# Kernel optimization log

Measured on AMD Instinct MI355X. Metric: run time of the kernel, lower is better.

## Reference

```python
import jax, jax.numpy as jnp
import numpy as np
import itertools, math

B, T, D = 4, 4096, 1024
H = 16
DIM = D // H          # 64
L, KB = 8, 4
R = 1 << KB           # 16
S = L * R             # 128
TOPK = 2


def setup_inputs() -> dict:
    key = jax.random.key(0)
    ks = jax.random.split(key, 8)
    x = jax.random.normal(ks[0], (B, T, D), dtype=jnp.float32)
    mask = jnp.ones((B, T), dtype=jnp.float32)
    sc = 1.0 / math.sqrt(D)
    Wq = jax.random.normal(ks[1], (D, D), dtype=jnp.float32) * sc
    Wk = jax.random.normal(ks[2], (D, D), dtype=jnp.float32) * sc
    Wv = jax.random.normal(ks[3], (D, D), dtype=jnp.float32) * sc
    Wout = jax.random.normal(ks[4], (D, D), dtype=jnp.float32) * sc
    b_out = jnp.zeros((D,), dtype=jnp.float32)
    # planes: (L, K_bits, head_dim) -> stored transposed as (head_dim, L*K_bits)
    planes = jax.random.normal(ks[5], (L * KB, DIM), dtype=jnp.float32)
    planes_T = planes.T
    # hypercube corners (R, K_bits) -> stored transposed as (K_bits, R)
    corners = jnp.asarray(list(itertools.product([-1.0, 1.0], repeat=KB)), dtype=jnp.float32)
    protos_T = corners.T
    logit_temp = jnp.zeros((), dtype=jnp.float32)  # log(1.0)
    return {"x": x, "mask": mask, "Wq": Wq, "Wk": Wk, "Wv": Wv,
            "Wout": Wout, "b_out": b_out, "planes_T": planes_T,
            "protos_T": protos_T, "logit_temp": logit_temp}


def reference(x, mask, Wq, Wk, Wv, Wout, b_out, planes_T, protos_T, logit_temp):
    b, t, d = x.shape
    Q = (x @ Wq).reshape(b, t, H, DIM)
    K = (x @ Wk).reshape(b, t, H, DIM)
    V = (x @ Wv).reshape(b, t, H, DIM)
    m = mask[:, :, None, None]
    Q, K, V = Q * m, K * m, V * m
    Q = jnp.transpose(Q, (0, 2, 1, 3))  # [B,H,T,dim]
    K = jnp.transpose(K, (0, 2, 1, 3))
    V = jnp.transpose(V, (0, 2, 1, 3))

    scale = jnp.clip(jnp.exp(logit_temp), 0.01, 20.0)
    # LSH hyperplane projections of K
    projK = jnp.einsum('bhtd,dp->bhtp', K, planes_T).reshape(b, H, t, L, KB)
    logitsK = jnp.einsum('bhtlk,kr->bhtlr', jnp.tanh(projK) / scale, protos_T)
    probsK = jax.nn.softmax(logitsK, axis=-1)  # [B,H,T,L,R]

    # top-k mask over R, then renormalize
    _, top_idx = jax.lax.top_k(probsK, TOPK)
    sel = jax.nn.one_hot(top_idx, R, dtype=probsK.dtype).sum(axis=-2)
    probsK = probsK * sel
    probsK = probsK / (probsK.sum(axis=-1, keepdims=True) + 1e-6)

    assign = probsK.reshape(b, H, t, S)  # [B,H,T,S]
    bucket_K = jnp.einsum('bhts,bhtd->bhsd', assign, K)
    bucket_V = jnp.einsum('bhts,bhtd->bhsd', assign, V)
    A = assign.sum(axis=2)[..., None]  # [B,H,S,1]
    bucket_K = bucket_K / (A + 1e-6)
    bucket_V = bucket_V / (A + 1e-6)

    scores = jnp.einsum('bhtd,bhsd->bhts', Q, bucket_K) / math.sqrt(DIM)
    probs_attn = jax.nn.softmax(scores, axis=-1)
    out = jnp.einsum('bhts,bhsd->bhtd', probs_attn, bucket_V)
    out = jnp.transpose(out, (0, 2, 1, 3)).reshape(b, t, d)
    return out @ Wout + b_out
```

## Files before the change

kernel.cpp:

```cpp
#include <hip/hip_runtime.h>
#include <math.h>
#include <stdint.h>

#define TT   4096
#define DD   1024
#define HH   16
#define DIMM 64
#define SS   128

typedef short bf16x8 __attribute__((ext_vector_type(8)));
typedef float f32x4  __attribute__((ext_vector_type(4)));

__device__ __forceinline__ unsigned short f2bf(float f) {
    uint32_t u = __float_as_uint(f);
    return (unsigned short)((u + 0x7fffu + ((u >> 16) & 1u)) >> 16);
}
__device__ __forceinline__ float bf2f(unsigned short h) {
    return __uint_as_float((uint32_t)h << 16);
}

#define GLD16(ldsp, gp) __builtin_amdgcn_global_load_lds( \
    (const __attribute__((address_space(1))) uint32_t*)(gp), \
    (__attribute__((address_space(3))) uint32_t*)(ldsp), 16, 0, 0)

__global__ __launch_bounds__(256) void cvt2_k(const float* __restrict__ x,
                                              unsigned short* __restrict__ xb,
                                              unsigned short* __restrict__ xlo)
{
    const size_t i = ((size_t)blockIdx.x * 256 + threadIdx.x) * 8;
    const float4 a = *(const float4*)&x[i];
    const float4 b = *(const float4*)&x[i + 4];
    const float v[8] = {a.x, a.y, a.z, a.w, b.x, b.y, b.z, b.w};
    unsigned short h[8], l[8];
#pragma unroll
    for (int j = 0; j < 8; j++) {
        h[j] = f2bf(v[j]);
        l[j] = f2bf(v[j] - bf2f(h[j]));
    }
    uint4 rh, rl;
    rh.x = (uint32_t)h[0] | ((uint32_t)h[1] << 16);
    rh.y = (uint32_t)h[2] | ((uint32_t)h[3] << 16);
    rh.z = (uint32_t)h[4] | ((uint32_t)h[5] << 16);
    rh.w = (uint32_t)h[6] | ((uint32_t)h[7] << 16);
    rl.x = (uint32_t)l[0] | ((uint32_t)l[1] << 16);
    rl.y = (uint32_t)l[2] | ((uint32_t)l[3] << 16);
    rl.z = (uint32_t)l[4] | ((uint32_t)l[5] << 16);
    rl.w = (uint32_t)l[6] | ((uint32_t)l[7] << 16);
    *(uint4*)&xb[i]  = rh;
    *(uint4*)&xlo[i] = rl;
}

__global__ __launch_bounds__(256) void tr_k(const float* __restrict__ W,
                                            unsigned short* __restrict__ WT)
{
    __shared__ unsigned short tile[32][33];
    const int bx = blockIdx.x * 32;
    const int by = blockIdx.y * 32;
    const int tx = threadIdx.x & 31, ty = threadIdx.x >> 5;
#pragma unroll
    for (int r = 0; r < 4; r++) {
        const int row = by + ty * 4 + r;
        tile[tx][ty * 4 + r] = f2bf(W[(size_t)row * 1024 + bx + tx]);
    }
    __syncthreads();
#pragma unroll
    for (int r = 0; r < 4; r++) {
        const int col = bx + ty * 4 + r;
        WT[(size_t)col * 1024 + by + tx] = tile[ty * 4 + r][tx];
    }
}

__global__ __launch_bounds__(256) void tr2_k(const float* __restrict__ Wp,
                                             unsigned short* __restrict__ WphT,
                                             unsigned short* __restrict__ WplT)
{
    __shared__ float tile[32][33];
    const int bx = blockIdx.x * 32;
    const int by = blockIdx.y * 32;
    const int tx = threadIdx.x & 31, ty = threadIdx.x >> 5;
#pragma unroll
    for (int r = 0; r < 4; r++) {
        const int row = by + ty * 4 + r;
        tile[tx][ty * 4 + r] = Wp[(size_t)row * 512 + bx + tx];
    }
    __syncthreads();
#pragma unroll
    for (int r = 0; r < 4; r++) {
        const int col = bx + ty * 4 + r;
        const float v = tile[ty * 4 + r][tx];
        const unsigned short hi = f2bf(v);
        const unsigned short lo = f2bf(v - bf2f(hi));
        WphT[(size_t)col * 1024 + by + tx] = hi;
        WplT[(size_t)col * 1024 + by + tx] = lo;
    }
}

__global__ __launch_bounds__(256) void qkv_k(
    const unsigned short* __restrict__ Abf, const unsigned short* __restrict__ BT,
    const float* __restrict__ mask, unsigned short* __restrict__ Qf,
    unsigned short* __restrict__ KVf)
{
    __shared__ short sMem[16384];
    short* sA = sMem;
    short* sB = sMem + 8192;
    const int tid = threadIdx.x;
    const int w  = tid >> 6;
    const int ln = tid & 63;
    const int wm = w & 1, wn = w >> 1;
    const int id   = blockIdx.y * 24 + blockIdx.x;
    const int xcd  = id & 7, kk = id >> 3;
    const int cg   = kk / 192, rem = kk % 192;
    const int band = xcd * 16 + rem / 12;
    const int colblk = cg * 12 + rem % 12;
    const int row0 = band * 128;
    const int col0 = colblk * 128;
    const int lr = ln >> 4, lc = ln & 15;

    f32x4 acc[4][4];
#pragma unroll
    for (int i = 0; i < 4; i++)
#pragma unroll
        for (int j = 0; j < 4; j++) acc[i][j] = (f32x4){0.f, 0.f, 0.f, 0.f};

    const int ia0 = 2 * w, ia1 = 2 * w + 1;
    const size_t gA0 = (size_t)(row0 + ia0 * 16 + lc) * 1024 + lr * 8;
    const size_t gA1 = (size_t)(row0 + ia1 * 16 + lc) * 1024 + lr * 8;
    const size_t gB0 = (size_t)(col0 + ia0 * 16 + lc) * 1024 + lr * 8;
    const size_t gB1 = (size_t)(col0 + ia1 * 16 + lc) * 1024 + lr * 8;

    auto STAGE = [&](int buf, int k0) {
        GLD16(&sA[buf * 4096 + ia0 * 512], Abf + gA0 + k0);
        GLD16(&sA[buf * 4096 + ia1 * 512], Abf + gA1 + k0);
        GLD16(&sB[buf * 4096 + ia0 * 512], BT  + gB0 + k0);
        GLD16(&sB[buf * 4096 + ia1 * 512], BT  + gB1 + k0);
    };

    STAGE(0, 0);
    __syncthreads();
    for (int t = 0; t < 32; t++) {
        const int cur = t & 1;
        if (t < 31) STAGE(cur ^ 1, (t + 1) * 32);
        bf16x8 af[4], bfr[4];
#pragma unroll
        for (int ib = 0; ib < 4; ib++)
            af[ib] = *(const bf16x8*)&sA[cur * 4096 + (wm * 4 + ib) * 512 + ln * 8];
#pragma unroll
        for (int jb = 0; jb < 4; jb++)
            bfr[jb] = *(const bf16x8*)&sB[cur * 4096 + (wn * 4 + jb) * 512 + ln * 8];
#pragma unroll
        for (int ib = 0; ib < 4; ib++)
#pragma unroll
            for (int jb = 0; jb < 4; jb++)
                acc[ib][jb] = __builtin_amdgcn_mfma_f32_16x16x32_bf16(
                    af[ib], bfr[jb], acc[ib][jb], 0, 0, 0);
        __syncthreads();
    }

    const int proj = colblk >> 3;
    const int b    = row0 >> 12;
    const int h0   = (colblk & 7) * 2;
    short* sT = sMem;

    if (proj == 0) {
#pragma unroll
        for (int ib = 0; ib < 4; ib++) {
#pragma unroll
            for (int r = 0; r < 4; r++) {
                const int tt = wm * 64 + ib * 16 + lr * 4 + r;
                const float mval = mask[row0 + tt];
#pragma unroll
                for (int jb = 0; jb < 4; jb++) {
                    const int d = jb * 16 + lc;
                    const int e = ((tt >> 4) * 2 + (d >> 5)) * 512 +
                                  ((tt & 15) + ((d >> 3) & 3) * 16) * 8 + (d & 7);
                    sT[wn * 8192 + e] = (short)f2bf(acc[ib][jb][r] * mval);
                }
            }
        }
        __syncthreads();
        const int tile = (row0 & (TT - 1)) >> 7;
#pragma unroll
        for (int i = 0; i < 8; i++) {
            const int flat = i * 256 + tid;
            const int h_l  = flat >> 10;
            const int off  = (flat & 1023) * 8;
            unsigned short* dst = Qf + (size_t)(b * HH + h0 + h_l) * 262144
                                + (size_t)tile * 8192 + off;
            *(uint4*)dst = *(const uint4*)&sT[h_l * 8192 + off];
        }
    } else {
        const int voff = (proj == 2) ? 4 : 0;
#pragma unroll
        for (int ib = 0; ib < 4; ib++) {
#pragma unroll
            for (int r = 0; r < 4; r++) {
                const int tt128 = wm * 64 + ib * 16 + lr * 4 + r;
                const float mval = mask[row0 + tt128];
                const int chunk = tt128 >> 6, tt6 = tt128 & 63;
                const int rbase = (wn * 2 + chunk) * 4096 +
                                  ((tt6 >> 3) & 3) * 128 + lc * 8 + (tt6 & 7);
                const int t5 = (tt6 >> 5) * 4 * 512;
#pragma unroll
                for (int jb = 0; jb < 4; jb++)
                    sT[rbase + t5 + jb * 512] = (short)f2bf(acc[ib][jb][r] * mval);
            }
        }
        __syncthreads();
        const int gc0 = (row0 & (TT - 1)) >> 6;
#pragma unroll
        for (int i = 0; i < 8; i++) {
            const int flat = i * 256 + tid;
            const int bf = flat >> 6;
            const int wi = flat & 63;
            const int h_l = bf >> 4, chunk = (bf >> 3) & 1;
            const int tt5 = (bf >> 2) & 1, nb = bf & 3;
            const int lidx = (h_l * 2 + chunk) * 4096 + (tt5 * 4 + nb) * 512 + wi * 8;
            const size_t gidx = (size_t)(b * HH + h0 + h_l) * 524288
                              + (size_t)(gc0 + chunk) * 8192
                              + (size_t)(tt5 * 8 + nb + voff) * 512 + wi * 8;
            *(uint4*)&KVf[gidx] = *(const uint4*)&sT[lidx];
        }
    }
}

__global__ __launch_bounds__(256) void out_k(
    const unsigned short* __restrict__ Abf, const unsigned short* __restrict__ BT,
    const float* __restrict__ bias, float* __restrict__ C)
{
    __shared__ short sA[2][4096];
    __shared__ short sB[2][4096];
    const int tid = threadIdx.x;
    const int w  = tid >> 6, ln = tid & 63;
    const int wm = w & 1, wn = w >> 1;
    const int id  = blockIdx.y * 8 + blockIdx.x;
    const int xcd = id & 7, kk = id >> 3;
    const int row0 = (xcd * 16 + (kk >> 3)) * 128;
    const int col0 = (kk & 7) * 128;
    const int lr = ln >> 4, lc = ln & 15;

    f32x4 acc[4][4];
#pragma unroll
    for (int i = 0; i < 4; i++)
#pragma unroll
        for (int j = 0; j < 4; j++) acc[i][j] = (f32x4){0.f, 0.f, 0.f, 0.f};

    const int ia0 = 2 * w, ia1 = 2 * w + 1;
    const size_t gA0 = (size_t)(row0 + ia0 * 16 + lc) * 1024 + lr * 8;
    const size_t gA1 = (size_t)(row0 + ia1 * 16 + lc) * 1024 + lr * 8;
    const size_t gB0 = (size_t)(col0 + ia0 * 16 + lc) * 1024 + lr * 8;
    const size_t gB1 = (size_t)(col0 + ia1 * 16 + lc) * 1024 + lr * 8;

    auto STAGE = [&](int buf, int k0) {
        GLD16(&sA[buf][ia0 * 512], Abf + gA0 + k0);
        GLD16(&sA[buf][ia1 * 512], Abf + gA1 + k0);
        GLD16(&sB[buf][ia0 * 512], BT  + gB0 + k0);
        GLD16(&sB[buf][ia1 * 512], BT  + gB1 + k0);
    };

    STAGE(0, 0);
    __syncthreads();
    for (int t = 0; t < 32; t++) {
        const int cur = t & 1;
        if (t < 31) STAGE(cur ^ 1, (t + 1) * 32);
        bf16x8 af[4], bfr[4];
#pragma unroll
        for (int ib = 0; ib < 4; ib++)
            af[ib] = *(const bf16x8*)&sA[cur][(wm * 4 + ib) * 512 + ln * 8];
#pragma unroll
        for (int jb = 0; jb < 4; jb++)
            bfr[jb] = *(const bf16x8*)&sB[cur][(wn * 4 + jb) * 512 + ln * 8];
#pragma unroll
        for (int ib = 0; ib < 4; ib++)
#pragma unroll
            for (int jb = 0; jb < 4; jb++)
                acc[ib][jb] = __builtin_amdgcn_mfma_f32_16x16x32_bf16(
                    af[ib], bfr[jb], acc[ib][jb], 0, 0, 0);
        __syncthreads();
    }

#pragma unroll
    for (int ib = 0; ib < 4; ib++) {
#pragma unroll
        for (int r = 0; r < 4; r++) {
            const int gr = row0 + wm * 64 + ib * 16 + lr * 4 + r;
#pragma unroll
            for (int jb = 0; jb < 4; jb++) {
                const int col = col0 + wn * 64 + jb * 16 + lc;
                C[(size_t)gr * 1024 + col] = acc[ib][jb][r] + bias[col];
            }
        }
    }
}

__global__ __launch_bounds__(256) void projm_k(
    const unsigned short* __restrict__ Ah, const unsigned short* __restrict__ Al,
    const unsigned short* __restrict__ Bh, const unsigned short* __restrict__ Bl,
    const float* __restrict__ mask, float* __restrict__ P)
{
    __shared__ short sAh[2][4096];
    __shared__ short sAl[2][4096];
    __shared__ short sBh[2][4096];
    __shared__ short sBl[2][4096];
    const int tid = threadIdx.x;
    const int w  = tid >> 6;
    const int ln = tid & 63;
    const int wm = w & 1, wn = w >> 1;
    const int id  = blockIdx.y * 4 + blockIdx.x;
    const int xcd = id & 7, kk = id >> 3;
    const int row0 = (xcd * 16 + (kk >> 2)) * 128;
    const int col0 = (kk & 3) * 128;
    const int lr = ln >> 4, lc = ln & 15;

    f32x4 acc[4][4];
#pragma unroll
    for (int i = 0; i < 4; i++)
#pragma unroll
        for (int j = 0; j < 4; j++) acc[i][j] = (f32x4){0.f, 0.f, 0.f, 0.f};

    const int ia0 = 2 * w, ia1 = 2 * w + 1;
    const size_t gA0 = (size_t)(row0 + ia0 * 16 + lc) * 1024 + lr * 8;
    const size_t gA1 = (size_t)(row0 + ia1 * 16 + lc) * 1024 + lr * 8;
    const size_t gB0 = (size_t)(col0 + ia0 * 16 + lc) * 1024 + lr * 8;
    const size_t gB1 = (size_t)(col0 + ia1 * 16 + lc) * 1024 + lr * 8;

    auto STAGE = [&](int buf, int k0) {
        GLD16(&sAh[buf][ia0 * 512], Ah + gA0 + k0);
        GLD16(&sAh[buf][ia1 * 512], Ah + gA1 + k0);
        GLD16(&sAl[buf][ia0 * 512], Al + gA0 + k0);
        GLD16(&sAl[buf][ia1 * 512], Al + gA1 + k0);
        GLD16(&sBh[buf][ia0 * 512], Bh + gB0 + k0);
        GLD16(&sBh[buf][ia1 * 512], Bh + gB1 + k0);
        GLD16(&sBl[buf][ia0 * 512], Bl + gB0 + k0);
        GLD16(&sBl[buf][ia1 * 512], Bl + gB1 + k0);
    };

    STAGE(0, 0);
    __syncthreads();
    for (int t = 0; t < 32; t++) {
        const int cur = t & 1;
        if (t < 31) STAGE(cur ^ 1, (t + 1) * 32);
        bf16x8 ah[4], al[4], bh[4], bl[4];
#pragma unroll
        for (int ib = 0; ib < 4; ib++) {
            ah[ib] = *(const bf16x8*)&sAh[cur][(wm * 4 + ib) * 512 + ln * 8];
            al[ib] = *(const bf16x8*)&sAl[cur][(wm * 4 + ib) * 512 + ln * 8];
        }
#pragma unroll
        for (int jb = 0; jb < 4; jb++) {
            bh[jb] = *(const bf16x8*)&sBh[cur][(wn * 4 + jb) * 512 + ln * 8];
            bl[jb] = *(const bf16x8*)&sBl[cur][(wn * 4 + jb) * 512 + ln * 8];
        }
#pragma unroll
        for (int ib = 0; ib < 4; ib++)
#pragma unroll
            for (int jb = 0; jb < 4; jb++) {
                acc[ib][jb] = __builtin_amdgcn_mfma_f32_16x16x32_bf16(
                    ah[ib], bh[jb], acc[ib][jb], 0, 0, 0);
                acc[ib][jb] = __builtin_amdgcn_mfma_f32_16x16x32_bf16(
                    ah[ib], bl[jb], acc[ib][jb], 0, 0, 0);
                acc[ib][jb] = __builtin_amdgcn_mfma_f32_16x16x32_bf16(
                    al[ib], bh[jb], acc[ib][jb], 0, 0, 0);
            }
        __syncthreads();
    }

#pragma unroll
    for (int ib = 0; ib < 4; ib++) {
#pragma unroll
        for (int r = 0; r < 4; r++) {
            const int gr = row0 + wm * 64 + ib * 16 + lr * 4 + r;
            const float mval = mask[gr];
            const int b = gr >> 12, t = gr & (TT - 1);
#pragma unroll
            for (int jb = 0; jb < 4; jb++) {
                const int c = col0 + wn * 64 + jb * 16 + lc;
                const int h = c >> 5, p = c & 31;
                P[(((size_t)(b * HH + h) * TT + t) * 32) + p] =
                    acc[ib][jb][r] * mval;
            }
        }
    }
}

__global__ __launch_bounds__(256) void wproj_k(
    const float* __restrict__ Wk, const float* __restrict__ planesT,
    float* __restrict__ Wp)
{
    __shared__ float sW[1024];
    __shared__ float sP[2048];
    const int tid = threadIdx.x;
    const int k = blockIdx.x;
    for (int i = tid; i < 1024; i += 256) sW[i] = Wk[(size_t)k * 1024 + i];
    for (int i = tid; i < 2048; i += 256) sP[i] = planesT[i];
    __syncthreads();
#pragma unroll
    for (int c0 = 0; c0 < 2; c0++) {
        const int c = c0 * 256 + tid;
        const int h = c >> 5, p = c & 31;
        float s = 0.f;
#pragma unroll
        for (int d = 0; d < 64; d++)
            s = fmaf(sW[h * 64 + d], sP[d * 32 + p], s);
        Wp[(size_t)k * 512 + c] = s;
    }
}

__global__ __launch_bounds__(256) void zero_k(float* __restrict__ p)
{
    const size_t i = ((size_t)blockIdx.x * 256 + threadIdx.x) * 4;
    *(float4*)&p[i] = make_float4(0.f, 0.f, 0.f, 0.f);
}

__global__ __launch_bounds__(256) void assign_k(
    const float* __restrict__ Pj, const float* __restrict__ protosT,
    const float* __restrict__ logit_temp,
    unsigned char* __restrict__ aIdx, float* __restrict__ aW,
    float* __restrict__ gA)
{
    __shared__ float sPr[4][16];
    __shared__ float sCnt[SS];
    const int tid = threadIdx.x;
    const int tc = blockIdx.x;
    const int bh = blockIdx.y;

    if (tid < 64)  ((float*)sPr)[tid] = protosT[tid];
    if (tid < SS)  sCnt[tid] = 0.f;
    __syncthreads();

    const float scale = fminf(fmaxf(__expf(logit_temp[0]), 0.01f), 20.0f);
    const float inv_scale = 1.0f / scale;

    const int t = tc * 256 + tid;
    const float* pr = Pj + ((size_t)bh * TT + t) * 32;
    float proj[32];
#pragma unroll
    for (int j = 0; j < 8; j++) {
        const float4 v = *(const float4*)&pr[j * 4];
        proj[j * 4 + 0] = v.x; proj[j * 4 + 1] = v.y;
        proj[j * 4 + 2] = v.z; proj[j * 4 + 3] = v.w;
    }
#pragma unroll
    for (int p = 0; p < 32; p++) proj[p] = tanhf(proj[p]) * inv_scale;

    unsigned char idx[16];
    float wv[16];
#pragma unroll
    for (int l = 0; l < 8; l++) {
        float g[16];
#pragma unroll
        for (int r = 0; r < 16; r++)
            g[r] = proj[l * 4 + 0] * sPr[0][r] + proj[l * 4 + 1] * sPr[1][r] +
                   proj[l * 4 + 2] * sPr[2][r] + proj[l * 4 + 3] * sPr[3][r];
        float mx = g[0];
#pragma unroll
        for (int r = 1; r < 16; r++) mx = fmaxf(mx, g[r]);
        float Zs = 0.f;
#pragma unroll
        for (int r = 0; r < 16; r++) Zs += __expf(g[r] - mx);
        int a = 0; float ga = g[0];
#pragma unroll
        for (int r = 1; r < 16; r++) { if (g[r] > ga) { ga = g[r]; a = r; } }
        int b2 = (a == 0) ? 1 : 0; float gb = g[b2];
#pragma unroll
        for (int r = 0; r < 16; r++) { if (r != a && g[r] > gb) { gb = g[r]; b2 = r; } }
        const float pa = __expf(ga - mx) / Zs;
        const float pb = __expf(gb - mx) / Zs;
        const float den = pa + pb + 1e-6f;
        const float wa = pa / den, wb = pb / den;
        idx[l * 2 + 0] = (unsigned char)(l * 16 + a);  wv[l * 2 + 0] = wa;
        idx[l * 2 + 1] = (unsigned char)(l * 16 + b2); wv[l * 2 + 1] = wb;
        atomicAdd(&sCnt[l * 16 + a],  wa);
        atomicAdd(&sCnt[l * 16 + b2], wb);
    }
    const size_t off = (size_t)bh * TT + t;
    uint32_t pk[4];
#pragma unroll
    for (int j = 0; j < 4; j++)
        pk[j] = (uint32_t)idx[j * 4] | ((uint32_t)idx[j * 4 + 1] << 8) |
                ((uint32_t)idx[j * 4 + 2] << 16) | ((uint32_t)idx[j * 4 + 3] << 24);
    *(uint4*)&aIdx[off * 16] = make_uint4(pk[0], pk[1], pk[2], pk[3]);
#pragma unroll
    for (int j = 0; j < 4; j++)
        *(float4*)&aW[off * 16 + j * 4] =
            make_float4(wv[j * 4], wv[j * 4 + 1], wv[j * 4 + 2], wv[j * 4 + 3]);
    __syncthreads();
    if (tid < SS) atomicAdd(&gA[bh * SS + tid], sCnt[tid]);
}

__global__ __launch_bounds__(256) void scatter4_k(
    const unsigned short* __restrict__ KVf,
    const unsigned char* __restrict__ aIdx, const float* __restrict__ aW,
    float* __restrict__ gBK, float* __restrict__ gBV)
{
    __shared__ short sA[8192];
    __shared__ short sB[8192];
    const int tid = threadIdx.x;
    const int tc = blockIdx.x;
    const int bh = blockIdx.y;
    const int w  = tid >> 6, ln = tid & 63;
    const int wm = w & 1, wn = w >> 1;

    f32x4 acc[4][4];
#pragma unroll
    for (int i = 0; i < 4; i++)
#pragma unroll
        for (int j = 0; j < 4; j++) acc[i][j] = (f32x4){0.f, 0.f, 0.f, 0.f};

    const size_t kvbase = (size_t)bh * 524288;
    const int ptt = tid >> 2, pg = tid & 3;

    for (int c = 0; c < 8; c++) {
        __syncthreads();
        const size_t cbase = kvbase + (size_t)(tc * 8 + c) * 8192;
#pragma unroll
        for (int i = 0; i < 4; i++) {
            const int seg = w * 4 + i;
            GLD16(&sB[seg * 512], KVf + cbase + seg * 512 + ln * 8);
        }
        {
            const uint4 z = make_uint4(0u, 0u, 0u, 0u);
#pragma unroll
            for (int r = 0; r < 4; r++)
                *(uint4*)&sA[(r * 256 + tid) * 8] = z;
        }
        __syncthreads();
        {
            const int t0 = tc * 512 + c * 64;
            const size_t off = (size_t)bh * TT + (t0 + ptt);
            const uint32_t pk = ((const uint32_t*)aIdx)[off * 4 + pg];
            const float4 wv = *(const float4*)&aW[off * 16 + pg * 4];
            const float w4[4] = {wv.x, wv.y, wv.z, wv.w};
#pragma unroll
            for (int q = 0; q < 4; q++) {
                const int s = (pk >> (8 * q)) & 255;
                sA[((ptt >> 5) * 8 + (s >> 4)) * 512 + ((ptt >> 3) & 3) * 128 +
                   (s & 15) * 8 + (ptt & 7)] = f2bf(w4[q]);
            }
        }
        __syncthreads();
#pragma unroll
        for (int ks = 0; ks < 2; ks++) {
            bf16x8 af[4], bfr[4];
#pragma unroll
            for (int ib = 0; ib < 4; ib++)
                af[ib] = *(const bf16x8*)&sA[(ks * 8 + wm * 4 + ib) * 512 + ln * 8];
#pragma unroll
            for (int jb = 0; jb < 4; jb++)
                bfr[jb] = *(const bf16x8*)&sB[(ks * 8 + wn * 4 + jb) * 512 + ln * 8];
#pragma unroll
            for (int ib = 0; ib < 4; ib++)
#pragma unroll
                for (int jb = 0; jb < 4; jb++)
                    acc[ib][jb] = __builtin_amdgcn_mfma_f32_16x16x32_bf16(
                        af[ib], bfr[jb], acc[ib][jb], 0, 0, 0);
        }
    }

    const int lr = ln >> 4, lc = ln & 15;
#pragma unroll
    for (int ib = 0; ib < 4; ib++) {
#pragma unroll
        for (int r = 0; r < 4; r++) {
            const int s = wm * 64 + ib * 16 + lr * 4 + r;
#pragma unroll
            for (int jb = 0; jb < 4; jb++) {
                const int col = wn * 64 + jb * 16 + lc;
                if (col < 64)
                    atomicAdd(&gBK[(size_t)bh * (SS * DIMM) + s * DIMM + col],
                              acc[ib][jb][r]);
                else
                    atomicAdd(&gBV[(size_t)bh * (SS * DIMM) + s * DIMM + (col - 64)],
                              acc[ib][jb][r]);
            }
        }
    }
}

__global__ __launch_bounds__(256) void bprep_k(
    const float* __restrict__ gBK, const float* __restrict__ gBV,
    const float* __restrict__ gA,
    unsigned short* __restrict__ Kf, unsigned short* __restrict__ VTf)
{
    __shared__ float sInv[SS];
    const int tid = threadIdx.x;
    const int bh = blockIdx.y;
    if (tid < SS) sInv[tid] = 1.0f / (gA[bh * SS + tid] + 1e-6f);
    __syncthreads();
#pragma unroll
    for (int it = 0; it < 8; it++) {
        const int i = (blockIdx.x * 8 + it) * 256 + tid;
        const int s = i >> 6, d = i & 63;
        const float kv = gBK[(size_t)bh * 8192 + i] * sInv[s];
        const float vv = gBV[(size_t)bh * 8192 + i] * sInv[s];
        const int ek = ((s >> 4) * 2 + (d >> 5)) * 512 +
                       ((s & 15) + ((d >> 3) & 3) * 16) * 8 + (d & 7);
        const int ev = ((d >> 4) * 4 + (s >> 5)) * 512 +
                       ((d & 15) + ((s >> 3) & 3) * 16) * 8 + (s & 7);
        Kf[(size_t)bh * 8192 + ek]  = f2bf(kv);
        VTf[(size_t)bh * 8192 + ev] = f2bf(vv);
    }
}

__global__ __launch_bounds__(256) void attn_m(
    const unsigned short* __restrict__ Qf, const unsigned short* __restrict__ Kf,
    const unsigned short* __restrict__ VTf, unsigned short* __restrict__ attb)
{
    __shared__ short sQ[8192];
    __shared__ short sK[8192];
    __shared__ short sVT[8192];
    __shared__ short sP[16384];
    const int tid = threadIdx.x;
    const int tc = blockIdx.x;
    const int bh = blockIdx.y;
    const int w = tid >> 6, l = tid & 63;

    const size_t qbase  = (size_t)bh * 262144 + (size_t)tc * 8192;
    const size_t kvbase = (size_t)bh * 8192;
#pragma unroll
    for (int i = 0; i < 4; i++) {
        const int o = (i * 256 + w * 64) * 8;
        GLD16(&sQ[o],  Qf  + qbase  + o + l * 8);
        GLD16(&sK[o],  Kf  + kvbase + o + l * 8);
        GLD16(&sVT[o], VTf + kvbase + o + l * 8);
    }
    __syncthreads();

    f32x4 acc[2][8];
#pragma unroll
    for (int i = 0; i < 2; i++)
#pragma unroll
        for (int j = 0; j < 8; j++) acc[i][j] = (f32x4){0.f, 0.f, 0.f, 0.f};

#pragma unroll
    for (int ks = 0; ks < 2; ks++) {
        const bf16x8 a0 = *(const bf16x8*)&sQ[((w * 2 + 0) * 2 + ks) * 512 + l * 8];
        const bf16x8 a1 = *(const bf16x8*)&sQ[((w * 2 + 1) * 2 + ks) * 512 + l * 8];
#pragma unroll
        for (int jb = 0; jb < 8; jb++) {
            const bf16x8 b = *(const bf16x8*)&sK[(jb * 2 + ks) * 512 + l * 8];
            acc[0][jb] = __builtin_amdgcn_mfma_f32_16x16x32_bf16(a0, b, acc[0][jb], 0, 0, 0);
            acc[1][jb] = __builtin_amdgcn_mfma_f32_16x16x32_bf16(a1, b, acc[1][jb], 0, 0, 0);
        }
    }

#pragma unroll
    for (int ib = 0; ib < 2; ib++) {
        const int mb = w * 2 + ib;
#pragma unroll
        for (int r = 0; r < 4; r++) {
            float v[8];
            float mx = -INFINITY;
#pragma unroll
            for (int jb = 0; jb < 8; jb++) {
                v[jb] = acc[ib][jb][r] * 0.125f;
                mx = fmaxf(mx, v[jb]);
            }
            mx = fmaxf(mx, __shfl_xor(mx, 1));
            mx = fmaxf(mx, __shfl_xor(mx, 2));
            mx = fmaxf(mx, __shfl_xor(mx, 4));
            mx = fmaxf(mx, __shfl_xor(mx, 8));
            float Z = 0.f;
#pragma unroll
            for (int jb = 0; jb < 8; jb++) { v[jb] = __expf(v[jb] - mx); Z += v[jb]; }
            Z += __shfl_xor(Z, 1);
            Z += __shfl_xor(Z, 2);
            Z += __shfl_xor(Z, 4);
            Z += __shfl_xor(Z, 8);
            const float invZ = 1.0f / Z;
            const int ttl = (l >> 4) * 4 + r;
#pragma unroll
            for (int jb = 0; jb < 8; jb++) {
                int e = (mb * 4 + (jb >> 1)) * 512 +
                        (ttl + (((jb * 2 + ((l >> 3) & 1)) & 3) * 16)) * 8 + (l & 7);
                e ^= ((e >> 7) & 3) << 4;
                sP[e] = (short)f2bf(v[jb] * invZ);
            }
        }
    }

    f32x4 acc2[2][4];
#pragma unroll
    for (int i = 0; i < 2; i++)
#pragma unroll
        for (int j = 0; j < 4; j++) acc2[i][j] = (f32x4){0.f, 0.f, 0.f, 0.f};

#pragma unroll
    for (int ks = 0; ks < 4; ks++) {
        bf16x8 a[2];
#pragma unroll
        for (int ib = 0; ib < 2; ib++) {
            int ia = ((w * 2 + ib) * 4 + ks) * 512 + l * 8;
            ia ^= ((ia >> 7) & 3) << 4;
            a[ib] = *(const bf16x8*)&sP[ia];
        }
#pragma unroll
        for (int jb = 0; jb < 4; jb++) {
            const bf16x8 b = *(const bf16x8*)&sVT[(jb * 4 + ks) * 512 + l * 8];
            acc2[0][jb] = __builtin_amdgcn_mfma_f32_16x16x32_bf16(a[0], b, acc2[0][jb], 0, 0, 0);
            acc2[1][jb] = __builtin_amdgcn_mfma_f32_16x16x32_bf16(a[1], b, acc2[1][jb], 0, 0, 0);
        }
    }

    const int b = bh >> 4, h = bh & 15;
#pragma unroll
    for (int ib = 0; ib < 2; ib++) {
#pragma unroll
        for (int r = 0; r < 4; r++) {
            const int t = tc * 128 + w * 32 + ib * 16 + (l >> 4) * 4 + r;
            unsigned short* outp = attb + ((size_t)(b * TT + t)) * DD + h * DIMM;
#pragma unroll
            for (int jb = 0; jb < 4; jb++)
                outp[jb * 16 + (l & 15)] = f2bf(acc2[ib][jb][r]);
        }
    }
}

extern "C" void kernel_launch(void* const* d_in, const int* in_sizes, int n_in,
                              void* d_out, int out_size, void* d_ws, size_t ws_size,
                              hipStream_t stream)
{
    const float* x       = (const float*)d_in[0];
    const float* mask    = (const float*)d_in[1];
    const float* Wq      = (const float*)d_in[2];
    const float* Wk      = (const float*)d_in[3];
    const float* Wv      = (const float*)d_in[4];
    const float* Wout    = (const float*)d_in[5];
    const float* b_out   = (const float*)d_in[6];
    const float* planesT = (const float*)d_in[7];
    const float* protosT = (const float*)d_in[8];
    const float* ltemp   = (const float*)d_in[9];
    float* out = (float*)d_out;

    float* ws  = (float*)d_ws;
    float* gBK = ws + (3u << 24);
    float* gBV = gBK + 524288;
    float* gA  = gBV + 524288;
    unsigned short* Qf    = (unsigned short*)ws;
    unsigned short* BTall = (unsigned short*)(ws + (1u << 24));
    unsigned short* KVf   = (unsigned short*)(ws + (2u << 24));
    unsigned short* xlo   = KVf;
    unsigned short* xb    = (unsigned short*)(ws + 51388416);
    float*          Wp    = ws;
    unsigned short* WphT  = (unsigned short*)(ws + 524288);
    unsigned short* WplT  = (unsigned short*)(ws + 786432);
    float*          aW    = ws + 51388416;
    unsigned char*  aIdx  = (unsigned char*)(ws + 55582720);
    unsigned short* Kf    = (unsigned short*)(ws + 56631296);
    unsigned short* VTf   = (unsigned short*)(ws + 56893440);
    unsigned short* attb  = KVf;
    unsigned short* WoutT = (unsigned short*)(ws + 41943040);
    float*          Pj    = (float*)d_out;

    const dim3 tg(32, 32);
    const dim3 t2g(16, 32);
    const dim3 pg(4, 128);
    const dim3 qg(24, 128);
    const dim3 og(8, 128);

    cvt2_k<<<8192, 256, 0, stream>>>(x, xb, xlo);

    wproj_k<<<1024, 256, 0, stream>>>(Wk, planesT, Wp);
    tr2_k<<<t2g, 256, 0, stream>>>(Wp, WphT, WplT);
    projm_k<<<pg, 256, 0, stream>>>(xb, xlo, WphT, WplT, mask, Pj);

    tr_k<<<tg, 256, 0, stream>>>(Wq, BTall);
    tr_k<<<tg, 256, 0, stream>>>(Wk, BTall + 1048576);
    tr_k<<<tg, 256, 0, stream>>>(Wv, BTall + 2097152);
    qkv_k<<<qg, 256, 0, stream>>>(xb, BTall, mask, Qf, KVf);

    zero_k<<<1032, 256, 0, stream>>>(gBK);
    assign_k<<<dim3(16, 64), 256, 0, stream>>>(Pj, protosT, ltemp, aIdx, aW, gA);
    scatter4_k<<<dim3(8, 64), 256, 0, stream>>>(KVf, aIdx, aW, gBK, gBV);

    bprep_k<<<dim3(4, 64), 256, 0, stream>>>(gBK, gBV, gA, Kf, VTf);
    tr_k<<<tg, 256, 0, stream>>>(Wout, WoutT);
    attn_m<<<dim3(32, 64), 256, 0, stream>>>(Qf, Kf, VTf, attb);

    out_k<<<og, 256, 0, stream>>>(attb, WoutT, b_out, out);
}
```

Measured before the change: 629.9 us.

## Triple-buffer GEMM LDS staging with partial vmcnt waits in qkv and out kernels

Replaces the double-buffered K-loop in the QKV and output projection GEMMs with a three-stage ring buffer. Two tiles are kept in flight, and each iteration waits only for the oldest loads (vmcnt(4)) followed by a raw s_barrier instead of a full __syncthreads. The goal is to hide more global-to-LDS latency behind the MFMA work. The cost is 48KB of LDS per block, which may lower occupancy, plus redundant dummy loads in the final iterations.

```diff
diff --git a/kernel.cpp b/kernel.cpp
--- a/kernel.cpp
+++ b/kernel.cpp
@@ -100,9 +100,7 @@
     const float* __restrict__ mask, unsigned short* __restrict__ Qf,
     unsigned short* __restrict__ KVf)
 {
-    __shared__ short sMem[16384];
-    short* sA = sMem;
-    short* sB = sMem + 8192;
+    __shared__ short sMem[24576];
     const int tid = threadIdx.x;
     const int w  = tid >> 6;
     const int ln = tid & 63;
@@ -129,32 +127,37 @@
     const size_t gB1 = (size_t)(col0 + ia1 * 16 + lc) * 1024 + lr * 8;
 
     auto STAGE = [&](int buf, int k0) {
-        GLD16(&sA[buf * 4096 + ia0 * 512], Abf + gA0 + k0);
-        GLD16(&sA[buf * 4096 + ia1 * 512], Abf + gA1 + k0);
-        GLD16(&sB[buf * 4096 + ia0 * 512], BT  + gB0 + k0);
-        GLD16(&sB[buf * 4096 + ia1 * 512], BT  + gB1 + k0);
+        short* bb = sMem + buf * 8192;
+        GLD16(&bb[ia0 * 512], Abf + gA0 + k0);
+        GLD16(&bb[ia1 * 512], Abf + gA1 + k0);
+        GLD16(&bb[4096 + ia0 * 512], BT + gB0 + k0);
+        GLD16(&bb[4096 + ia1 * 512], BT + gB1 + k0);
     };
 
     STAGE(0, 0);
-    __syncthreads();
+    STAGE(1, 32);
+    asm volatile("s_waitcnt vmcnt(4)" ::: "memory");
+    __builtin_amdgcn_s_barrier();
     for (int t = 0; t < 32; t++) {
-        const int cur = t & 1;
-        if (t < 31) STAGE(cur ^ 1, (t + 1) * 32);
+        STAGE((t + 2) % 3, (t + 2 < 32) ? (t + 2) * 32 : 0);
+        const short* bb = sMem + (t % 3) * 8192;
         bf16x8 af[4], bfr[4];
 #pragma unroll
         for (int ib = 0; ib < 4; ib++)
-            af[ib] = *(const bf16x8*)&sA[cur * 4096 + (wm * 4 + ib) * 512 + ln * 8];
+            af[ib] = *(const bf16x8*)&bb[(wm * 4 + ib) * 512 + ln * 8];
 #pragma unroll
         for (int jb = 0; jb < 4; jb++)
-            bfr[jb] = *(const bf16x8*)&sB[cur * 4096 + (wn * 4 + jb) * 512 + ln * 8];
+            bfr[jb] = *(const bf16x8*)&bb[4096 + (wn * 4 + jb) * 512 + ln * 8];
 #pragma unroll
         for (int ib = 0; ib < 4; ib++)
 #pragma unroll
             for (int jb = 0; jb < 4; jb++)
                 acc[ib][jb] = __builtin_amdgcn_mfma_f32_16x16x32_bf16(
                     af[ib], bfr[jb], acc[ib][jb], 0, 0, 0);
-        __syncthreads();
-    }
+        asm volatile("s_waitcnt vmcnt(4)" ::: "memory");
+        __builtin_amdgcn_s_barrier();
+    }
+    __syncthreads();
 
     const int proj = colblk >> 3;
     const int b    = row0 >> 12;
@@ -227,8 +230,7 @@
     const unsigned short* __restrict__ Abf, const unsigned short* __restrict__ BT,
     const float* __restrict__ bias, float* __restrict__ C)
 {
-    __shared__ short sA[2][4096];
-    __shared__ short sB[2][4096];
+    __shared__ short sMem[24576];
     const int tid = threadIdx.x;
     const int w  = tid >> 6, ln = tid & 63;
     const int wm = w & 1, wn = w >> 1;
@@ -251,31 +253,35 @@
     const size_t gB1 = (size_t)(col0 + ia1 * 16 + lc) * 1024 + lr * 8;
 
     auto STAGE = [&](int buf, int k0) {
-        GLD16(&sA[buf][ia0 * 512], Abf + gA0 + k0);
-        GLD16(&sA[buf][ia1 * 512], Abf + gA1 + k0);
-        GLD16(&sB[buf][ia0 * 512], BT  + gB0 + k0);
-        GLD16(&sB[buf][ia1 * 512], BT  + gB1 + k0);
+        short* bb = sMem + buf * 8192;
+        GLD16(&bb[ia0 * 512], Abf + gA0 + k0);
+        GLD16(&bb[ia1 * 512], Abf + gA1 + k0);
+        GLD16(&bb[4096 + ia0 * 512], BT + gB0 + k0);
+        GLD16(&bb[4096 + ia1 * 512], BT + gB1 + k0);
     };
 
     STAGE(0, 0);
-    __syncthreads();
+    STAGE(1, 32);
+    asm volatile("s_waitcnt vmcnt(4)" ::: "memory");
+    __builtin_amdgcn_s_barrier();
     for (int t = 0; t < 32; t++) {
-        const int cur = t & 1;
-        if (t < 31) STAGE(cur ^ 1, (t + 1) * 32);
+        STAGE((t + 2) % 3, (t + 2 < 32) ? (t + 2) * 32 : 0);
+        const short* bb = sMem + (t % 3) * 8192;
         bf16x8 af[4], bfr[4];
 #pragma unroll
         for (int ib = 0; ib < 4; ib++)
-            af[ib] = *(const bf16x8*)&sA[cur][(wm * 4 + ib) * 512 + ln * 8];
+            af[ib] = *(const bf16x8*)&bb[(wm * 4 + ib) * 512 + ln * 8];
 #pragma unroll
         for (int jb = 0; jb < 4; jb++)
-            bfr[jb] = *(const bf16x8*)&sB[cur][(wn * 4 + jb) * 512 + ln * 8];
+            bfr[jb] = *(const bf16x8*)&bb[4096 + (wn * 4 + jb) * 512 + ln * 8];
 #pragma unroll
         for (int ib = 0; ib < 4; ib++)
 #pragma unroll
             for (int jb = 0; jb < 4; jb++)
                 acc[ib][jb] = __builtin_amdgcn_mfma_f32_16x16x32_bf16(
                     af[ib], bfr[jb], acc[ib][jb], 0, 0, 0);
-        __syncthreads();
+        asm volatile("s_waitcnt vmcnt(4)" ::: "memory");
+        __builtin_amdgcn_s_barrier();
     }
 
 #pragma unroll
```

Result: faster. 617.2 us (-2.0%).
